# Kernel tuning notes

Measured on AMD Instinct MI355X. Metric: run time of the kernel, lower is better.

The kernel has to match this reference:

```python
import jax, jax.numpy as jnp
import numpy as np
from jax import lax


def _heaviside(x):
    return (jnp.tanh(5.0 * x) + 1.0) / 2.0


def _soilbucket(s1, pet, f, smax, qmax):
    f = (f + 1.0) / 20.0
    smax = (smax + 1.0) * 700.0 + 100.0
    qmax = (qmax + 1.0) * 20.0 + 10.0
    hs1 = _heaviside(s1)
    over = _heaviside(s1 - smax)
    under = _heaviside(smax - s1)
    et = hs1 * over * pet + hs1 * under * pet * (s1 / smax)
    qsub = hs1 * over * qmax + hs1 * under * qmax * jnp.exp(-f * (smax - s1))
    qsurf = hs1 * over * (s1 - smax)
    return et, qsub, qsurf


def setup_inputs() -> dict:
    key = jax.random.key(0)
    k1, k2, k3, k4 = jax.random.split(key, 4)
    B, T, A, H = 4096, 2000, 27, 32
    forcing = jax.random.uniform(k1, (B, T, 5), dtype=jnp.float32) * 10.0
    attrs = jax.random.normal(k2, (B, A), dtype=jnp.float32)
    w1 = jax.random.uniform(k3, (A, H), minval=-0.05, maxval=0.05, dtype=jnp.float32)
    b1 = jnp.zeros((H,), jnp.float32)
    w2 = jax.random.uniform(k4, (H, 6), minval=-0.05, maxval=0.05, dtype=jnp.float32)
    b2 = jnp.zeros((6,), jnp.float32)
    return {"forcing": forcing, "attrs": attrs, "w1": w1, "b1": b1, "w2": w2, "b2": b2}


def reference(forcing, attrs, w1, b1, w2, b2):
    # forcing: [B,T,5]; attrs: [B,27]
    prcp = forcing[:, :, 0]   # [B,T]
    tmean = forcing[:, :, 1]
    dayl = forcing[:, :, 2]
    # Hamon PET
    pet = 29.8 * (dayl * 24.0) * 0.611 * jnp.exp(17.3 * tmean / (tmean + 237.3)) / (tmean + 273.2)

    # parameterization MLP -> 6 physical parameters in [-1,1]
    h = jnp.tanh(attrs @ w1 + b1)
    paras = jnp.tanh(h @ w2 + b2)        # [B,6]
    tmin_r, tmax_r, ddf_r, f_r, smax_r, qmax_r = [paras[:, i] for i in range(6)]

    # pre-transform per-sample constants used inside the step
    tmin = (tmin_r + 1.0) * -1.5
    tmax = (tmax_r + 1.0) * 1.5
    ddf = (ddf_r + 1.0) * 2.5

    B = forcing.shape[0]

    def step(carry, x):
        s0, s1 = carry           # [B], [B]
        p, t, pet_t = x          # [B] each
        psnow = _heaviside(tmin - t) * p
        prain = _heaviside(t - tmin) * p
        melt = _heaviside(t - tmax) * _heaviside(s0) * jnp.minimum(s0, ddf * (t - tmax))
        et, qsub, qsurf = _soilbucket(s1, pet_t, f_r, smax_r, qmax_r)
        ds0 = psnow - melt
        ds1 = prain + melt - et - qsub - qsurf
        ns0 = s0 + jnp.clip(ds0, -1e5, 1e5)
        ns1 = s1 + jnp.clip(ds1, -1e5, 1e5)
        return (ns0, ns1), ns1

    xs = (prcp.T, tmean.T, pet.T)  # [T,B] each
    init = (jnp.zeros((B,), forcing.dtype), jnp.zeros((B,), forcing.dtype))
    _, s1_seq = lax.scan(step, init, xs)   # s1_seq: [T,B]
    s1_seq = s1_seq.T                       # [B,T]

    _, qsub, qsurf = _soilbucket(s1_seq, pet, f_r[:, None], smax_r[:, None], qmax_r[:, None])
    return (qsub + qsurf)[..., None]        # [B,T,1]
```

## Files before the change

kernel.cpp:

```cpp
#include <hip/hip_runtime.h>
#include <math.h>

__device__ __forceinline__ float hv(float x) {
    return __builtin_amdgcn_rcpf(1.0f + __expf(-10.0f * x));
}

__global__ void params_kernel(const float* __restrict__ attrs,
                              const float* __restrict__ w1,
                              const float* __restrict__ b1,
                              const float* __restrict__ w2,
                              const float* __restrict__ b2,
                              float* __restrict__ params, int B) {
    int b = blockIdx.x * blockDim.x + threadIdx.x;
    if (b >= B) return;
    float a[27];
#pragma unroll
    for (int i = 0; i < 27; ++i) a[i] = attrs[b * 27 + i];
    float h[32];
#pragma unroll
    for (int j = 0; j < 32; ++j) {
        float s = b1[j];
#pragma unroll
        for (int i = 0; i < 27; ++i) s = fmaf(a[i], w1[i * 32 + j], s);
        h[j] = tanhf(s);
    }
    float p[6];
#pragma unroll
    for (int k = 0; k < 6; ++k) {
        float s = b2[k];
#pragma unroll
        for (int j = 0; j < 32; ++j) s = fmaf(h[j], w2[j * 6 + k], s);
        p[k] = tanhf(s);
    }
    float tmin = (p[0] + 1.0f) * -1.5f;
    float tmax = (p[1] + 1.0f) * 1.5f;
    float ddf  = (p[2] + 1.0f) * 2.5f;
    float f    = (p[3] + 1.0f) / 20.0f;
    float smax = (p[4] + 1.0f) * 700.0f + 100.0f;
    float qmax = (p[5] + 1.0f) * 20.0f + 10.0f;
    params[0 * B + b] = tmin;
    params[1 * B + b] = tmax;
    params[2 * B + b] = ddf;
    params[3 * B + b] = f;
    params[4 * B + b] = smax;
    params[5 * B + b] = qmax;
    params[6 * B + b] = 1.0f / smax;
}

__global__ __launch_bounds__(256)
void prep_kernel(const float* __restrict__ forcing,
                 const float* __restrict__ params,
                 float4* __restrict__ qv,
                 float* __restrict__ petT,
                 int B, int T) {
    __shared__ float raw[64][165];
    int b0 = blockIdx.x * 64, t0 = blockIdx.y * 32;
    size_t total4 = ((size_t)B * T * 5) >> 2;
    for (int idx = threadIdx.x; idx < 64 * 40; idx += 256) {
        int row = idx / 40, quad = idx - row * 40;
        size_t f4 = ((((size_t)(b0 + row) * T + t0) * 5) >> 2) + quad;
        float4 v = make_float4(0.f, 0.f, 0.f, 0.f);
        if (f4 < total4) v = ((const float4*)forcing)[f4];
        raw[row][quad * 4 + 0] = v.x;
        raw[row][quad * 4 + 1] = v.y;
        raw[row][quad * 4 + 2] = v.z;
        raw[row][quad * 4 + 3] = v.w;
    }
    __syncthreads();
    int bl = threadIdx.x & 63;
    int b = b0 + bl;
    float tmin = params[0 * B + b], tmax = params[1 * B + b], ddf = params[2 * B + b];
    for (int tt = threadIdx.x >> 6; tt < 32; tt += 4) {
        int t = t0 + tt;
        if (t >= T) break;
        float p  = raw[bl][tt * 5 + 0];
        float tm = raw[bl][tt * 5 + 1];
        float dl = raw[bl][tt * 5 + 2];
        float pet = 29.8f * (dl * 24.0f) * 0.611f
                    * __expf(17.3f * tm / (tm + 237.3f)) / (tm + 273.2f);
        float psnow = hv(tmin - tm) * p;
        float prain = p - psnow;
        float dt2 = tm - tmax;
        float Hm1 = hv(dt2);
        float M = Hm1 * (ddf * dt2);
        qv[(size_t)t * B + b] = make_float4(psnow, prain, Hm1, M);
        petT[(size_t)t * B + b] = pet;
    }
}

#define STEP(q, pt)                                                     \
    {                                                                   \
        float Hs0  = hv(s0);                                            \
        float melt = Hs0 * fminf((q).z * s0, (q).w);                    \
        float hs1  = hv(s1);                                            \
        float d    = s1 - smax;                                         \
        float over = hv(d);                                             \
        float ex   = __expf(f * d);                                     \
        float A    = (pt) + qmax + d;                                   \
        float Bv   = fmaf((pt) * ism, s1, qmax * ex);                   \
        float loss = hs1 * fmaf(over, A - Bv, Bv);                      \
        float ds0  = (q).x - melt;                                      \
        float ds1  = (q).y + melt - loss;                               \
        s0 += fminf(fmaxf(ds0, -100000.0f), 100000.0f);                 \
        s1 += fminf(fmaxf(ds1, -100000.0f), 100000.0f);                 \
    }

__global__ __launch_bounds__(64, 1)
void scan_kernel(const float4* __restrict__ qv,
                 const float* __restrict__ petT,
                 const float* __restrict__ params,
                 float* __restrict__ s1T,
                 int B, int T) {
    int b = blockIdx.x * 64 + threadIdx.x;
    float f    = params[3 * B + b];
    float smax = params[4 * B + b];
    float qmax = params[5 * B + b];
    float ism  = params[6 * B + b];
    float s0 = 0.0f, s1 = 0.0f;
    constexpr int LOOK = 16;
    float4 a[LOOK];
    float pe[LOOK];
    const float4* pq = qv + b;
    const float*  pp = petT + b;
    float*        ps = s1T + b;
    const size_t strideC = (size_t)LOOK * B;
#pragma unroll
    for (int j = 0; j < LOOK; ++j) {
        a[j]  = pq[(size_t)j * B];
        pe[j] = pp[(size_t)j * B];
    }
    int nFull = T / LOOK;
    for (int c = 0; c < nFull - 1; ++c) {
#pragma unroll
        for (int j = 0; j < LOOK; ++j) {
            float4 q = a[j];
            float pt = pe[j];
            a[j]  = pq[(size_t)(j + LOOK) * B];
            pe[j] = pp[(size_t)(j + LOOK) * B];
            STEP(q, pt);
            ps[(size_t)j * B] = s1;
        }
        pq += strideC; pp += strideC; ps += strideC;
    }
#pragma unroll
    for (int j = 0; j < LOOK; ++j) {
        float4 q = a[j];
        float pt = pe[j];
        STEP(q, pt);
        ps[(size_t)j * B] = s1;
    }
    pq += strideC; pp += strideC; ps += strideC;
    for (int i = 0; i < T - nFull * LOOK; ++i) {
        float4 q = pq[(size_t)i * B];
        float pt = pp[(size_t)i * B];
        STEP(q, pt);
        ps[(size_t)i * B] = s1;
    }
}

__global__ void out_kernel(const float* __restrict__ s1T,
                           const float* __restrict__ params,
                           float* __restrict__ out,
                           int B, int T) {
    __shared__ float lq[64][65];
    int b0 = blockIdx.x * 64, t0 = blockIdx.y * 64;
    {
        int bl = threadIdx.x & 63;
        int b = b0 + bl;
        float f    = params[3 * B + b];
        float smax = params[4 * B + b];
        float qmax = params[5 * B + b];
        for (int tt = threadIdx.x >> 6; tt < 64; tt += 4) {
            int t = t0 + tt;
            int tv = (t < T) ? t : (T - 1);
            float s1 = s1T[(size_t)tv * B + b];
            float hs1   = hv(s1);
            float dd    = s1 - smax;
            float over  = hv(dd);
            float under = 1.0f - over;
            float qs    = hs1 * qmax;
            float qsub  = qs * over + qs * under * __expf(f * dd);
            float qsurf = hs1 * over * dd;
            lq[tt][bl] = qsub + qsurf;
        }
    }
    __syncthreads();
    {
        int tl = threadIdx.x & 63;
        int t = t0 + tl;
        if (t < T) {
            for (int bb = threadIdx.x >> 6; bb < 64; bb += 4) {
                out[(size_t)(b0 + bb) * T + t] = lq[tl][bb];
            }
        }
    }
}

extern "C" void kernel_launch(void* const* d_in, const int* in_sizes, int n_in,
                              void* d_out, int out_size, void* d_ws, size_t ws_size,
                              hipStream_t stream) {
    const float* forcing = (const float*)d_in[0];
    const float* attrs   = (const float*)d_in[1];
    const float* w1      = (const float*)d_in[2];
    const float* b1      = (const float*)d_in[3];
    const float* w2      = (const float*)d_in[4];
    const float* b2      = (const float*)d_in[5];
    float* out = (float*)d_out;

    int B = in_sizes[1] / 27;
    int T = in_sizes[0] / (B * 5);

    char* ws = (char*)d_ws;
    size_t off = 0;
    float4* qv   = (float4*)(ws + off); off += (size_t)B * T * sizeof(float4);
    float* petT  = (float*)(ws + off);  off += (size_t)B * T * sizeof(float);
    float* s1T   = (float*)(ws + off);  off += (size_t)B * T * sizeof(float);
    float* params = (float*)(ws + off); off += (size_t)7 * B * sizeof(float);

    params_kernel<<<(B + 255) / 256, 256, 0, stream>>>(attrs, w1, b1, w2, b2, params, B);
    dim3 g2(B / 64, (T + 31) / 32);
    prep_kernel<<<g2, 256, 0, stream>>>(forcing, params, qv, petT, B, T);
    scan_kernel<<<B / 64, 64, 0, stream>>>(qv, petT, params, s1T, B, T);
    dim3 g4(B / 64, (T + 63) / 64);
    out_kernel<<<g4, 256, 0, stream>>>(s1T, params, out, B, T);
}
```

Measured before the change: 508.6 us.

## Fuse output computation into scan kernel with LDS double-buffered async loads

Removes the separate output kernel and the s1T intermediate buffer by computing qsub+qsurf inside the scan from the previous state and writing 16 consecutive outputs per lane as float4 stores. Forcing data is now staged through a double-buffered LDS ring filled with global_load_lds instead of a register lookahead. The step math is rewritten with exp2 and a single combined reciprocal for the two heaviside terms. Each lane writes a strided row of the output, so stores are uncoalesced across the wave, and the scan still runs only 64 single-wave blocks.

```diff
diff --git a/kernel.cpp b/kernel.cpp
--- a/kernel.cpp
+++ b/kernel.cpp
@@ -1,8 +1,20 @@
 #include <hip/hip_runtime.h>
 #include <math.h>
+#include <stdint.h>
 
 __device__ __forceinline__ float hv(float x) {
     return __builtin_amdgcn_rcpf(1.0f + __expf(-10.0f * x));
+}
+
+__device__ __forceinline__ void gload16(const void* g, void* l) {
+    __builtin_amdgcn_global_load_lds(
+        (const __attribute__((address_space(1))) uint32_t*)g,
+        (__attribute__((address_space(3))) uint32_t*)l, 16, 0, 0);
+}
+__device__ __forceinline__ void gload4(const void* g, void* l) {
+    __builtin_amdgcn_global_load_lds(
+        (const __attribute__((address_space(1))) uint32_t*)g,
+        (__attribute__((address_space(3))) uint32_t*)l, 4, 0, 0);
 }
 
 __global__ void params_kernel(const float* __restrict__ attrs,
@@ -45,6 +57,7 @@
     params[4 * B + b] = smax;
     params[5 * B + b] = qmax;
     params[6 * B + b] = 1.0f / smax;
+    params[7 * B + b] = f * 1.4426950408889634f;
 }
 
 __global__ __launch_bounds__(256)
@@ -88,112 +101,152 @@
     }
 }
 
-#define STEP(q, pt)                                                     \
-    {                                                                   \
-        float Hs0  = hv(s0);                                            \
-        float melt = Hs0 * fminf((q).z * s0, (q).w);                    \
-        float hs1  = hv(s1);                                            \
-        float d    = s1 - smax;                                         \
-        float over = hv(d);                                             \
-        float ex   = __expf(f * d);                                     \
-        float A    = (pt) + qmax + d;                                   \
-        float Bv   = fmaf((pt) * ism, s1, qmax * ex);                   \
-        float loss = hs1 * fmaf(over, A - Bv, Bv);                      \
-        float ds0  = (q).x - melt;                                      \
-        float ds1  = (q).y + melt - loss;                               \
-        s0 += fminf(fmaxf(ds0, -100000.0f), 100000.0f);                 \
-        s1 += fminf(fmaxf(ds1, -100000.0f), 100000.0f);                 \
-    }
-
 __global__ __launch_bounds__(64, 1)
 void scan_kernel(const float4* __restrict__ qv,
                  const float* __restrict__ petT,
                  const float* __restrict__ params,
-                 float* __restrict__ s1T,
+                 float* __restrict__ out,
                  int B, int T) {
-    int b = blockIdx.x * 64 + threadIdx.x;
-    float f    = params[3 * B + b];
-    float smax = params[4 * B + b];
-    float qmax = params[5 * B + b];
-    float ism  = params[6 * B + b];
+    __shared__ float4 ldsQ[2][16][64];
+    __shared__ float  ldsP[2][16][64];
+    int lane = threadIdx.x;
+    int b = blockIdx.x * 64 + lane;
+    if (b >= B) return;
+    const float smax = params[4 * B + b];
+    const float qmax = params[5 * B + b];
+    const float ism  = params[6 * B + b];
+    const float fl2  = params[7 * B + b];
+    const float C10  = -14.426950408889634f;
+    const size_t bT = (size_t)b * T;
     float s0 = 0.0f, s1 = 0.0f;
-    constexpr int LOOK = 16;
-    float4 a[LOOK];
-    float pe[LOOK];
-    const float4* pq = qv + b;
-    const float*  pp = petT + b;
-    float*        ps = s1T + b;
-    const size_t strideC = (size_t)LOOK * B;
-#pragma unroll
-    for (int j = 0; j < LOOK; ++j) {
-        a[j]  = pq[(size_t)j * B];
-        pe[j] = pp[(size_t)j * B];
-    }
-    int nFull = T / LOOK;
-    for (int c = 0; c < nFull - 1; ++c) {
-#pragma unroll
-        for (int j = 0; j < LOOK; ++j) {
-            float4 q = a[j];
-            float pt = pe[j];
-            a[j]  = pq[(size_t)(j + LOOK) * B];
-            pe[j] = pp[(size_t)(j + LOOK) * B];
-            STEP(q, pt);
-            ps[(size_t)j * B] = s1;
-        }
-        pq += strideC; pp += strideC; ps += strideC;
-    }
-#pragma unroll
-    for (int j = 0; j < LOOK; ++j) {
-        float4 q = a[j];
-        float pt = pe[j];
-        STEP(q, pt);
-        ps[(size_t)j * B] = s1;
-    }
-    pq += strideC; pp += strideC; ps += strideC;
-    for (int i = 0; i < T - nFull * LOOK; ++i) {
-        float4 q = pq[(size_t)i * B];
-        float pt = pp[(size_t)i * B];
-        STEP(q, pt);
-        ps[(size_t)i * B] = s1;
-    }
-}
-
-__global__ void out_kernel(const float* __restrict__ s1T,
-                           const float* __restrict__ params,
-                           float* __restrict__ out,
-                           int B, int T) {
-    __shared__ float lq[64][65];
-    int b0 = blockIdx.x * 64, t0 = blockIdx.y * 64;
+    float obuf[16];
+    float qq_last = 0.0f;
+
+    auto flush16 = [&](int start) {
+        if (((bT + (size_t)start) & 3) == 0) {
+            float4* dst = (float4*)(out + bT + start);
+            dst[0] = make_float4(obuf[0],  obuf[1],  obuf[2],  obuf[3]);
+            dst[1] = make_float4(obuf[4],  obuf[5],  obuf[6],  obuf[7]);
+            dst[2] = make_float4(obuf[8],  obuf[9],  obuf[10], obuf[11]);
+            dst[3] = make_float4(obuf[12], obuf[13], obuf[14], obuf[15]);
+        } else {
+#pragma unroll
+            for (int i = 0; i < 16; ++i) out[bT + start + i] = obuf[i];
+        }
+    };
+
+#define STEP_MATH(q, pt)                                                  \
+    {                                                                     \
+        float e0   = exp2f(C10 * s0);                                     \
+        float Hs0  = __builtin_amdgcn_rcpf(1.0f + e0);                    \
+        float melt = Hs0 * fminf((q).z * s0, (q).w);                      \
+        float d    = s1 - smax;                                           \
+        float a1   = fminf(C10 * s1, 63.0f);                              \
+        float a2   = fminf(C10 * d, 63.0f);                               \
+        float e1   = exp2f(a1);                                           \
+        float e2   = exp2f(a2);                                           \
+        float r    = __builtin_amdgcn_rcpf((1.0f + e1) * (1.0f + e2));    \
+        float ex   = exp2f(fl2 * d);                                      \
+        float qex  = qmax * ex;                                           \
+        float qd   = qmax + d;                                            \
+        float A    = (pt) + qd;                                           \
+        float Bv   = fmaf((pt) * ism, s1, qex);                           \
+        float loss = r * fmaf(e2, Bv, A);                                 \
+        qq_last    = r * fmaf(e2, qex, qd);                               \
+        float ds0  = (q).x - melt;                                        \
+        float ds1  = ((q).y + melt) - loss;                               \
+        s0 += __builtin_amdgcn_fmed3f(ds0, -100000.0f, 100000.0f);        \
+        s1 += __builtin_amdgcn_fmed3f(ds1, -100000.0f, 100000.0f);        \
+    }
+
+    int nFull = T / 16;
+    int cur = 0;
+    if (nFull > 0) {
+        {
+            const float4* qs = qv + b;
+            const float*  ps = petT + b;
+#pragma unroll
+            for (int j = 0; j < 16; ++j) {
+                gload16(qs + (size_t)j * B, &ldsQ[0][j][0]);
+                gload4 (ps + (size_t)j * B, &ldsP[0][j][0]);
+            }
+        }
+        asm volatile("s_waitcnt vmcnt(0)" ::: "memory");
+        __builtin_amdgcn_sched_barrier(0);
+
+        for (int c = 0; c < nFull - 1; ++c) {
+            {
+                const float4* qs = qv + ((size_t)(c + 1) * 16) * B + b;
+                const float*  ps = petT + ((size_t)(c + 1) * 16) * B + b;
+                int nxt = cur ^ 1;
+#pragma unroll
+                for (int j = 0; j < 16; ++j) {
+                    gload16(qs + (size_t)j * B, &ldsQ[nxt][j][0]);
+                    gload4 (ps + (size_t)j * B, &ldsP[nxt][j][0]);
+                }
+            }
+            __builtin_amdgcn_sched_barrier(0);
+            int t0 = 16 * c;
+            bool doflush = (c > 0);
+#pragma unroll
+            for (int j = 0; j < 16; ++j) {
+                float4 q = ldsQ[cur][j][lane];
+                float pt = ldsP[cur][j][lane];
+                STEP_MATH(q, pt);
+                if (j == 0) {
+                    if (doflush) { obuf[15] = qq_last; flush16(t0 - 16); }
+                } else {
+                    obuf[j - 1] = qq_last;
+                }
+            }
+            asm volatile("s_waitcnt vmcnt(0)" ::: "memory");
+            __builtin_amdgcn_sched_barrier(0);
+            cur ^= 1;
+        }
+        {
+            int t0 = 16 * (nFull - 1);
+            bool doflush = (nFull > 1);
+#pragma unroll
+            for (int j = 0; j < 16; ++j) {
+                float4 q = ldsQ[cur][j][lane];
+                float pt = ldsP[cur][j][lane];
+                STEP_MATH(q, pt);
+                if (j == 0) {
+                    if (doflush) { obuf[15] = qq_last; flush16(t0 - 16); }
+                } else {
+                    obuf[j - 1] = qq_last;
+                }
+            }
+        }
+    }
+    for (int t = nFull * 16; t < T; ++t) {
+        float4 q = qv[(size_t)t * B + b];
+        float pt = petT[(size_t)t * B + b];
+        STEP_MATH(q, pt);
+        if ((t & 15) == 0) {
+            if (t > 0) { obuf[15] = qq_last; flush16(t - 16); }
+        } else {
+            out[bT + (t - 1)] = qq_last;
+        }
+    }
     {
-        int bl = threadIdx.x & 63;
-        int b = b0 + bl;
-        float f    = params[3 * B + b];
-        float smax = params[4 * B + b];
-        float qmax = params[5 * B + b];
-        for (int tt = threadIdx.x >> 6; tt < 64; tt += 4) {
-            int t = t0 + tt;
-            int tv = (t < T) ? t : (T - 1);
-            float s1 = s1T[(size_t)tv * B + b];
-            float hs1   = hv(s1);
-            float dd    = s1 - smax;
-            float over  = hv(dd);
-            float under = 1.0f - over;
-            float qs    = hs1 * qmax;
-            float qsub  = qs * over + qs * under * __expf(f * dd);
-            float qsurf = hs1 * over * dd;
-            lq[tt][bl] = qsub + qsurf;
-        }
-    }
-    __syncthreads();
-    {
-        int tl = threadIdx.x & 63;
-        int t = t0 + tl;
-        if (t < T) {
-            for (int bb = threadIdx.x >> 6; bb < 64; bb += 4) {
-                out[(size_t)(b0 + bb) * T + t] = lq[tl][bb];
-            }
-        }
-    }
+        float d   = s1 - smax;
+        float a1  = fminf(C10 * s1, 63.0f);
+        float a2  = fminf(C10 * d, 63.0f);
+        float e1  = exp2f(a1);
+        float e2  = exp2f(a2);
+        float r   = __builtin_amdgcn_rcpf((1.0f + e1) * (1.0f + e2));
+        float ex  = exp2f(fl2 * d);
+        float qex = qmax * ex;
+        float qd  = qmax + d;
+        float qqf = r * fmaf(e2, qex, qd);
+        if ((T & 15) == 0) {
+            if (T > 0) { obuf[15] = qqf; flush16(T - 16); }
+        } else {
+            out[bT + (T - 1)] = qqf;
+        }
+    }
+#undef STEP_MATH
 }
 
 extern "C" void kernel_launch(void* const* d_in, const int* in_sizes, int n_in,
@@ -214,13 +267,10 @@
     size_t off = 0;
     float4* qv   = (float4*)(ws + off); off += (size_t)B * T * sizeof(float4);
     float* petT  = (float*)(ws + off);  off += (size_t)B * T * sizeof(float);
-    float* s1T   = (float*)(ws + off);  off += (size_t)B * T * sizeof(float);
-    float* params = (float*)(ws + off); off += (size_t)7 * B * sizeof(float);
+    float* params = (float*)(ws + off); off += (size_t)8 * B * sizeof(float);
 
     params_kernel<<<(B + 255) / 256, 256, 0, stream>>>(attrs, w1, b1, w2, b2, params, B);
     dim3 g2(B / 64, (T + 31) / 32);
     prep_kernel<<<g2, 256, 0, stream>>>(forcing, params, qv, petT, B, T);
-    scan_kernel<<<B / 64, 64, 0, stream>>>(qv, petT, params, s1T, B, T);
-    dim3 g4(B / 64, (T + 63) / 64);
-    out_kernel<<<g4, 256, 0, stream>>>(s1T, params, out, B, T);
-}
+    scan_kernel<<<(B + 63) / 64, 64, 0, stream>>>(qv, petT, params, out, B, T);
+}
```

After: 605.8 us. +19.1%, slower.
